# Kernel optimization log

Measured on AMD Instinct MI355X. Metric: run time of the kernel, lower is better.

Reference implementation:

```python
import jax, jax.numpy as jnp
import numpy as np

N_E = 8192
E_DIM = 256
BETA = 0.25


def setup_inputs() -> dict:
    key = jax.random.key(0)
    kz, ke = jax.random.split(key)
    z = jax.random.normal(kz, (16, E_DIM, 32, 32), dtype=jnp.float32)
    embedding = jax.random.uniform(ke, (N_E, E_DIM), dtype=jnp.float32,
                                   minval=-1.0 / N_E, maxval=1.0 / N_E)
    return {"z": z, "embedding": embedding}


def reference(z, embedding):
    n_e, e_dim = embedding.shape
    # (B, C, H, W) -> (B, H, W, C) -> (N, e_dim)
    zp = jnp.transpose(z, (0, 2, 3, 1))
    zf = zp.reshape(-1, e_dim)
    # squared L2 distances: |z|^2 + |e|^2 - 2 z.e   -> (N, n_e)
    dists = (jnp.sum(zf * zf, axis=1, keepdims=True)
             + jnp.sum(embedding * embedding, axis=1)
             - 2.0 * (zf @ embedding.T))
    # two smallest distances (top-2 of negated dists)
    _, top2_idx = jax.lax.top_k(-dists, 2)
    min_encoding_indices = top2_idx[:, 0:1]
    second_encoding_indices = top2_idx[:, 1:2]
    min_encodings = jax.nn.one_hot(top2_idx[:, 0], n_e, dtype=zp.dtype)  # (N, n_e)
    z_q = (min_encodings @ embedding).reshape(zp.shape)
    # commitment / codebook loss
    loss = (jnp.mean((jax.lax.stop_gradient(z_q) - zp) ** 2)
            + BETA * jnp.mean((z_q - jax.lax.stop_gradient(zp)) ** 2))
    # straight-through estimator
    z_q = zp + jax.lax.stop_gradient(z_q - zp)
    avg_probs = jnp.mean(min_encodings, axis=0)
    perplexity = jnp.exp(-jnp.sum(avg_probs * jnp.log(avg_probs + 1e-10)))
    z_q = jnp.transpose(z_q, (0, 3, 1, 2))
    return (loss, z_q, perplexity, min_encodings,
            min_encoding_indices, second_encoding_indices)
```

## Files before the change

kernel.cpp:

```cpp
#include <hip/hip_runtime.h>
#include <cfloat>
#include <cstdint>
#include <cstddef>

#define M_ROWS 16384
#define NE     8192
#define KD     256

#define OFF_LOSS   0ULL
#define OFF_ZQ     1ULL
#define OFF_PERP   4194305ULL
#define OFF_ONEHOT 4194306ULL
#define OFF_I0     138412034ULL
#define OFF_I1     138428418ULL

#define SCR_Z16  0ULL
#define SCR_E16  2097152ULL
#define SCR_PART 3145728ULL

#define WS_I0    0
#define WS_HIST  16384
#define WS_ENORM 24576
#define WS_CNORM 32768
#define WS_T0SUM 49152
#define WS_TOTAL 49154

typedef _Float16 fp16x8 __attribute__((ext_vector_type(8)));
typedef float    floatx16 __attribute__((ext_vector_type(16)));

__device__ __forceinline__ void async_load16(const void* g, void* lds) {
    __builtin_amdgcn_global_load_lds(
        (const __attribute__((address_space(1))) void*)g,
        (__attribute__((address_space(3))) void*)lds, 16, 0, 0);
}

__global__ void zero_ws_kernel(float* __restrict__ ws) {
    int i = blockIdx.x * 256 + threadIdx.x;
    if (i < WS_TOTAL) ws[i] = 0.0f;
}

__global__ void zero_onehot_kernel(float* __restrict__ out) {
    size_t tidg = (size_t)blockIdx.x * 1024 + threadIdx.x;
    float4* base = (float4*)(out + OFF_ONEHOT + 2);
    const float4 zz = make_float4(0.f, 0.f, 0.f, 0.f);
#pragma unroll
    for (int i = 0; i < 8; i++) {
        size_t q = tidg + (size_t)i * 4194304ULL;
        if (q < 33554431ULL) base[q] = zz;
    }
    if (tidg == 0) {
        out[OFF_ONEHOT + 0] = 0.f;
        out[OFF_ONEHOT + 1] = 0.f;
        out[OFF_ONEHOT + 134217726ULL] = 0.f;
        out[OFF_ONEHOT + 134217727ULL] = 0.f;
    }
}

__global__ void scatter_ones_kernel(const int* __restrict__ ws_i0, float* __restrict__ out) {
    int r = blockIdx.x * 256 + threadIdx.x;
    int j = ws_i0[r] & (NE - 1);
    out[OFF_ONEHOT + (size_t)r * NE + j] = 1.0f;
}

__device__ __forceinline__ float pairwise16(const float* sq, int lane16) {
    const int h = lane16 >> 3;
    const int j = lane16 & 7;
    float r = sq[h * 128 + j];
#pragma unroll
    for (int i = 1; i < 16; i++) r = r + sq[h * 128 + i * 8 + j];
    float s = r + __shfl_xor(r, 1);
    s = s + __shfl_xor(s, 2);
    s = s + __shfl_xor(s, 4);
    s = s + __shfl_xor(s, 8);
    return s;
}

__global__ void enorm_kernel(const float* __restrict__ emb, float* __restrict__ enorm) {
    __shared__ float sq[16][257];
    const int tid = threadIdx.x;
    const int row0 = blockIdx.x * 16;
#pragma unroll
    for (int p = 0; p < 4; p++) {
        int q = p * 256 + tid;
        int rl = q >> 6, kq = q & 63;
        float4 v = *(const float4*)(emb + (size_t)(row0 + rl) * KD + kq * 4);
        sq[rl][kq * 4 + 0] = v.x * v.x;
        sq[rl][kq * 4 + 1] = v.y * v.y;
        sq[rl][kq * 4 + 2] = v.z * v.z;
        sq[rl][kq * 4 + 3] = v.w * v.w;
    }
    __syncthreads();
    const int rl = tid >> 4, lane16 = tid & 15;
    float s = pairwise16(&sq[rl][0], lane16);
    if (lane16 == 0) enorm[row0 + rl] = s;
}

__global__ void cnorm_kernel(const float* __restrict__ z, float* __restrict__ cnorm) {
    __shared__ float sq[16][257];
    const int tid = threadIdx.x;
    const int r0  = blockIdx.x * 16;
    const int b   = r0 >> 10;
    const int hw0 = r0 & 1023;
    const float* zb = z + ((size_t)b << 18) + hw0;
#pragma unroll
    for (int p = 0; p < 4; p++) {
        int q = p * 256 + tid;
        int c = q >> 2, hq = q & 3;
        float4 v = *(const float4*)(zb + ((size_t)c << 10) + hq * 4);
        sq[hq * 4 + 0][c] = v.x * v.x;
        sq[hq * 4 + 1][c] = v.y * v.y;
        sq[hq * 4 + 2][c] = v.z * v.z;
        sq[hq * 4 + 3][c] = v.w * v.w;
    }
    __syncthreads();
    const int rl = tid >> 4, lane16 = tid & 15;
    float s = pairwise16(&sq[rl][0], lane16);
    if (lane16 == 0) cnorm[r0 + rl] = s;
}

__global__ void split_z_kernel(const float* __restrict__ z, _Float16* __restrict__ z16) {
    __shared__ float tile[64][65];
    const int tid = threadIdx.x;
    const int r0  = blockIdx.x * 64;
    const int kb  = blockIdx.y;
    const int b   = r0 >> 10;
    const int hw0 = r0 & 1023;
#pragma unroll
    for (int p = 0; p < 4; p++) {
        int q = p * 256 + tid;
        int cl = q >> 4, hq = q & 15;
        float4 v = *(const float4*)(z + ((size_t)b << 18) + (size_t)(kb * 64 + cl) * 1024 + hw0 + hq * 4);
        tile[hq * 4 + 0][cl] = v.x;
        tile[hq * 4 + 1][cl] = v.y;
        tile[hq * 4 + 2][cl] = v.z;
        tile[hq * 4 + 3][cl] = v.w;
    }
    __syncthreads();
#pragma unroll
    for (int p = 0; p < 2; p++) {
        int u = p * 256 + tid;
        int row = u >> 3, k8 = u & 7;
        int r = r0 + row;
        fp16x8 vh;
#pragma unroll
        for (int e = 0; e < 8; e++) vh[e] = (_Float16)tile[row][k8 * 8 + e];
        size_t unit = ((size_t)(r >> 7) * 4 + kb) * 1024 + (size_t)(r & 127) * 8 + (k8 ^ (r & 7));
        *(fp16x8*)(z16 + unit * 8) = vh;
    }
}

__global__ void split_e_kernel(const float* __restrict__ emb, _Float16* __restrict__ e16) {
    int u = blockIdx.x * 256 + threadIdx.x;
    size_t go = (size_t)u * 8;
    float4 v0 = *(const float4*)(emb + go);
    float4 v1 = *(const float4*)(emb + go + 4);
    float x[8] = {v0.x, v0.y, v0.z, v0.w, v1.x, v1.y, v1.z, v1.w};
    fp16x8 vh;
#pragma unroll
    for (int e = 0; e < 8; e++) vh[e] = (_Float16)(x[e] * 256.0f);
    int code = u >> 5, kc = (u >> 3) & 3, ku8 = u & 7;
    int kj = ku8 ^ (code & 7);
    size_t unit = ((size_t)(code >> 7) * 4 + kc) * 1024 + (size_t)(code & 127) * 8 + kj;
    *(fp16x8*)(e16 + unit * 8) = vh;
}

__device__ __forceinline__ void stage16k(_Float16* lds, const _Float16* gsrc,
                                         int wid, int lane) {
#pragma unroll
    for (int p = 0; p < 4; p++) {
        int u = p * 256 + wid * 64;
        async_load16((const void*)(gsrc + (size_t)(u + lane) * 8),
                     (void*)(lds + (size_t)u * 8));
    }
}

__device__ __forceinline__ fp16x8 frag_ld(const _Float16* lds, int rc, int ku) {
    int slot = rc * 8 + (ku ^ (rc & 7));
    return *(const fp16x8*)(lds + slot * 8);
}

#define MFMA(d, a, b) d = __builtin_amdgcn_mfma_f32_32x32x16_f16(a, b, d, 0, 0, 0)

__device__ __forceinline__ bool lex_lt(float t, int i, float T, int I) {
    return (t < T) || (t == T && i < I);
}

__device__ __forceinline__ void ins4(float t, int i,
    float& t0, int& i0, float& t1, int& i1,
    float& t2, int& i2, float& t3, int& i3) {
    if (lex_lt(t, i, t3, i3)) {
        if (lex_lt(t, i, t2, i2)) {
            t3 = t2; i3 = i2;
            if (lex_lt(t, i, t1, i1)) {
                t2 = t1; i2 = i1;
                if (lex_lt(t, i, t0, i0)) { t1 = t0; i1 = i0; t0 = t; i0 = i; }
                else { t1 = t; i1 = i; }
            } else { t2 = t; i2 = i; }
        } else { t3 = t; i3 = i; }
    }
}

__launch_bounds__(256, 2)
__global__ void mfma_top4_kernel(const _Float16* __restrict__ e16, const _Float16* __restrict__ z16,
                                 const float* __restrict__ enorm_g, const float* __restrict__ cnorm_g,
                                 float4* __restrict__ part) {
    __shared__ _Float16 As[2][8192];
    __shared__ _Float16 Bs[2][8192];
    __shared__ float en_all[1024];
    __shared__ float mbuf[128][8];

    const int tid = threadIdx.x;
    const int lane = tid & 63, wid = tid >> 6;
    const int l31 = lane & 31, half = lane >> 5;
    const int wave_m = wid & 1, wave_n = wid >> 1;
    const int zb = blockIdx.x, jg = blockIdx.y;
    const int brow0 = zb * 128;

    const int rcA0 = wave_m * 64 + l31, rcA1 = rcA0 + 32;
    const int rcB0 = wave_n * 64 + l31, rcB1 = rcB0 + 32;

#pragma unroll
    for (int p = 0; p < 4; p++) en_all[p * 256 + tid] = enorm_g[jg * 1024 + p * 256 + tid];

    float Cn[2];
    Cn[0] = cnorm_g[brow0 + wave_n * 64 + l31];
    Cn[1] = cnorm_g[brow0 + wave_n * 64 + 32 + l31];

    float q0[2], q1[2], q2[2], q3[2];
    int   j0[2], j1[2], j2[2], j3[2];
#pragma unroll
    for (int s = 0; s < 2; s++) {
        q0[s] = q1[s] = q2[s] = q3[s] = FLT_MAX;
        j0[s] = j1[s] = j2[s] = j3[s] = 0x7fffffff;
    }

    stage16k(As[0], e16 + ((size_t)((jg * 8 + 0) * 4 + 0) * 1024) * 8, wid, lane);
    stage16k(Bs[0], z16 + ((size_t)(zb * 4 + 0) * 1024) * 8, wid, lane);
    __syncthreads();

    floatx16 acc00, acc01, acc10, acc11;
    for (int iter = 0; iter < 32; iter++) {
        const int jt = iter >> 2, kc = iter & 3;
        const int cur = iter & 1;
        if (kc == 0) {
            acc00 = (floatx16)0.f; acc01 = (floatx16)0.f;
            acc10 = (floatx16)0.f; acc11 = (floatx16)0.f;
        }
        if (iter < 31) {
            const int ni = iter + 1, njt = ni >> 2, nkc = ni & 3;
            stage16k(As[cur ^ 1], e16 + ((size_t)((jg * 8 + njt) * 4 + nkc) * 1024) * 8, wid, lane);
            stage16k(Bs[cur ^ 1], z16 + ((size_t)(zb * 4 + nkc) * 1024) * 8, wid, lane);
        }
#pragma unroll
        for (int ks = 0; ks < 4; ks++) {
            const int ku = ks * 2 + half;
            fp16x8 a0 = frag_ld(As[cur], rcA0, ku);
            fp16x8 a1 = frag_ld(As[cur], rcA1, ku);
            fp16x8 b0 = frag_ld(Bs[cur], rcB0, ku);
            fp16x8 b1 = frag_ld(Bs[cur], rcB1, ku);
            MFMA(acc00, a0, b0);
            MFMA(acc01, a0, b1);
            MFMA(acc10, a1, b0);
            MFMA(acc11, a1, b1);
        }
        if (kc == 3) {
            const int jbase = jg * 1024 + jt * 128;
#pragma unroll
            for (int a = 0; a < 2; a++) {
#pragma unroll
                for (int reg = 0; reg < 16; reg++) {
                    const int rl = (reg & 3) + 8 * (reg >> 2) + 4 * half;
                    const int cl = wave_m * 64 + a * 32 + rl;
                    const int code = jbase + cl;
                    const float E = en_all[jt * 128 + cl];
                    float g0 = (a == 0) ? acc00[reg] : acc10[reg];
                    float g1 = (a == 0) ? acc01[reg] : acc11[reg];
                    float ta = fmaf(-0.0078125f, g0, Cn[0] + E);
                    ins4(ta, code, q0[0], j0[0], q1[0], j1[0], q2[0], j2[0], q3[0], j3[0]);
                    float tb = fmaf(-0.0078125f, g1, Cn[1] + E);
                    ins4(tb, code, q0[1], j0[1], q1[1], j1[1], q2[1], j2[1], q3[1], j3[1]);
                }
            }
        }
        __syncthreads();
    }

#pragma unroll
    for (int s = 0; s < 2; s++) {
        float ot0 = __shfl_xor(q0[s], 32), ot1 = __shfl_xor(q1[s], 32),
              ot2 = __shfl_xor(q2[s], 32), ot3 = __shfl_xor(q3[s], 32);
        int oi0 = __shfl_xor(j0[s], 32), oi1 = __shfl_xor(j1[s], 32),
            oi2 = __shfl_xor(j2[s], 32), oi3 = __shfl_xor(j3[s], 32);
        ins4(ot0, oi0, q0[s], j0[s], q1[s], j1[s], q2[s], j2[s], q3[s], j3[s]);
        ins4(ot1, oi1, q0[s], j0[s], q1[s], j1[s], q2[s], j2[s], q3[s], j3[s]);
        ins4(ot2, oi2, q0[s], j0[s], q1[s], j1[s], q2[s], j2[s], q3[s], j3[s]);
        ins4(ot3, oi3, q0[s], j0[s], q1[s], j1[s], q2[s], j2[s], q3[s], j3[s]);
    }

    __syncthreads();
    if (wave_m == 1 && lane < 32) {
#pragma unroll
        for (int s = 0; s < 2; s++) {
            int zr = wave_n * 64 + s * 32 + l31;
            mbuf[zr][0] = q0[s]; mbuf[zr][1] = q1[s]; mbuf[zr][2] = q2[s]; mbuf[zr][3] = q3[s];
            mbuf[zr][4] = __int_as_float(j0[s]); mbuf[zr][5] = __int_as_float(j1[s]);
            mbuf[zr][6] = __int_as_float(j2[s]); mbuf[zr][7] = __int_as_float(j3[s]);
        }
    }
    __syncthreads();
    if (wave_m == 0 && lane < 32) {
#pragma unroll
        for (int s = 0; s < 2; s++) {
            int zr = wave_n * 64 + s * 32 + l31;
            ins4(mbuf[zr][0], __float_as_int(mbuf[zr][4]),
                 q0[s], j0[s], q1[s], j1[s], q2[s], j2[s], q3[s], j3[s]);
            ins4(mbuf[zr][1], __float_as_int(mbuf[zr][5]),
                 q0[s], j0[s], q1[s], j1[s], q2[s], j2[s], q3[s], j3[s]);
            ins4(mbuf[zr][2], __float_as_int(mbuf[zr][6]),
                 q0[s], j0[s], q1[s], j1[s], q2[s], j2[s], q3[s], j3[s]);
            ins4(mbuf[zr][3], __float_as_int(mbuf[zr][7]),
                 q0[s], j0[s], q1[s], j1[s], q2[s], j2[s], q3[s], j3[s]);
            float4 pa = make_float4(q0[s], q1[s], q2[s], q3[s]);
            float4 pb = make_float4(__int_as_float(j0[s]), __int_as_float(j1[s]),
                                    __int_as_float(j2[s]), __int_as_float(j3[s]));
            size_t base = ((size_t)(brow0 + zr) * 8 + jg) * 2;
            part[base] = pa;
            part[base + 1] = pb;
        }
    }
}

__global__ void rescore_kernel(const float* __restrict__ z, const float* __restrict__ emb,
                               const float* __restrict__ enorm_g, const float* __restrict__ cnorm_g,
                               const float4* __restrict__ part, float* __restrict__ out,
                               int* __restrict__ ws_i0, int* __restrict__ hist,
                               double* __restrict__ t0sum) {
    const int tid  = threadIdx.x;
    const int lane = tid & 63, wid = tid >> 6;
    const int r = blockIdx.x * 4 + wid;
    const int b = r >> 10, hw = r & 1023;
    const float* zb = z + ((size_t)b << 18) + hw;

    const int c4 = lane * 4;
    const double zv0 = (double)zb[(size_t)(c4 + 0) << 10];
    const double zv1 = (double)zb[(size_t)(c4 + 1) << 10];
    const double zv2 = (double)zb[(size_t)(c4 + 2) << 10];
    const double zv3 = (double)zb[(size_t)(c4 + 3) << 10];

    float m1 = FLT_MAX, m2 = FLT_MAX;
    for (int jg = 0; jg < 8; jg++) {
        float4 pa = part[((size_t)r * 8 + jg) * 2];
        if (pa.x < m1) { m2 = m1; m1 = pa.x; } else if (pa.x < m2) m2 = pa.x;
        if (pa.y < m1) { m2 = m1; m1 = pa.y; } else if (pa.y < m2) m2 = pa.y;
    }
    const float T = m2 + 1.2e-4f;
    const float C = cnorm_g[r];

    float bt0 = FLT_MAX, bt1 = FLT_MAX;
    int   bi0 = NE - 1, bi1 = NE - 1;
    bool  any = false;
    for (int jg = 0; jg < 8; jg++) {
        float4 pa = part[((size_t)r * 8 + jg) * 2];
        float4 pb = part[((size_t)r * 8 + jg) * 2 + 1];
        float tv[4] = {pa.x, pa.y, pa.z, pa.w};
        int   jv[4] = {__float_as_int(pb.x), __float_as_int(pb.y),
                       __float_as_int(pb.z), __float_as_int(pb.w)};
        for (int e = 0; e < 4; e++) {
            if (tv[e] <= T) {
                const int j = jv[e] & (NE - 1);
                const float* er = emb + ((size_t)j << 8);
                float4 ev = *(const float4*)(er + c4);
                double gl = zv0 * (double)ev.x + zv1 * (double)ev.y +
                            zv2 * (double)ev.z + zv3 * (double)ev.w;
#pragma unroll
                for (int m = 1; m < 64; m <<= 1) gl += __shfl_xor(gl, m);
                float g2 = (float)(2.0 * gl);
                float S = C + enorm_g[j];
                float tex = S - g2;
                if (tex < bt0 || (tex == bt0 && j < bi0)) {
                    bt1 = bt0; bi1 = bi0; bt0 = tex; bi0 = j;
                } else if (tex < bt1 || (tex == bt1 && j < bi1)) {
                    bt1 = tex; bi1 = j;
                }
                any = true;
            }
        }
    }
    if (!any) { bt0 = 0.f; bi0 = 0; bi1 = 0; }

    if (lane == 0) {
        out[OFF_I0 + r] = (float)bi0;
        out[OFF_I1 + r] = (float)bi1;
        ws_i0[r] = bi0;
        atomicAdd(&hist[bi0], 1);
    }
    __shared__ double red[4];
    if (lane == 0) red[wid] = (double)bt0;
    __syncthreads();
    if (tid == 0) atomicAdd(t0sum, (red[0] + red[1]) + (red[2] + red[3]));
}

__global__ void zq_kernel(const float* __restrict__ emb, const int* __restrict__ ws_i0,
                          float* __restrict__ out) {
    int bc = blockIdx.x;
    int bb = bc >> 8, c = bc & 255;
    int hwb = threadIdx.x * 4;
    const int4 iv = *(const int4*)(ws_i0 + bb * 1024 + hwb);
    float* op = out + OFF_ZQ + ((size_t)bc << 10) + hwb;
    op[0] = emb[(size_t)(iv.x & (NE - 1)) * KD + c];
    op[1] = emb[(size_t)(iv.y & (NE - 1)) * KD + c];
    op[2] = emb[(size_t)(iv.z & (NE - 1)) * KD + c];
    op[3] = emb[(size_t)(iv.w & (NE - 1)) * KD + c];
}

__global__ void finalize_kernel(const int* __restrict__ hist, const double* __restrict__ t0sum,
                                float* __restrict__ out) {
    __shared__ float red[256];
    float s = 0.f;
    for (int j = threadIdx.x; j < NE; j += 256) {
        float p = (float)hist[j] * (1.0f / 16384.0f);
        s += p * logf(p + 1e-10f);
    }
    red[threadIdx.x] = s;
    __syncthreads();
    for (int m = 128; m; m >>= 1) {
        if (threadIdx.x < m) red[threadIdx.x] += red[threadIdx.x + m];
        __syncthreads();
    }
    if (threadIdx.x == 0) {
        out[OFF_PERP] = expf(-red[0]);
        out[OFF_LOSS] = 1.25f * (float)(t0sum[0] * (1.0 / 4194304.0));
    }
}

extern "C" void kernel_launch(void* const* d_in, const int* in_sizes, int n_in,
                              void* d_out, int out_size, void* d_ws, size_t ws_size,
                              hipStream_t stream) {
    const float* z   = (const float*)d_in[0];
    const float* emb = (const float*)d_in[1];
    float* out = (float*)d_out;
    float* ws  = (float*)d_ws;

    int*    ws_i0    = (int*)ws + WS_I0;
    int*    ws_hist  = (int*)ws + WS_HIST;
    float*  ws_enorm = ws + WS_ENORM;
    float*  ws_cnorm = ws + WS_CNORM;
    double* ws_t0sum = (double*)(ws + WS_T0SUM);

    float* scr = out + OFF_ONEHOT + 2;
    _Float16* z16 = (_Float16*)(scr + SCR_Z16);
    _Float16* e16 = (_Float16*)(scr + SCR_E16);
    float4* part = (float4*)(scr + SCR_PART);

    hipLaunchKernelGGL(zero_ws_kernel, dim3(194), dim3(256), 0, stream, ws);
    hipLaunchKernelGGL(enorm_kernel, dim3(512), dim3(256), 0, stream, emb, ws_enorm);
    hipLaunchKernelGGL(cnorm_kernel, dim3(1024), dim3(256), 0, stream, z, ws_cnorm);
    hipLaunchKernelGGL(split_z_kernel, dim3(256, 4), dim3(256), 0, stream, z, z16);
    hipLaunchKernelGGL(split_e_kernel, dim3(1024), dim3(256), 0, stream, emb, e16);
    hipLaunchKernelGGL(mfma_top4_kernel, dim3(128, 8), dim3(256), 0, stream,
                       e16, z16, ws_enorm, ws_cnorm, part);
    hipLaunchKernelGGL(rescore_kernel, dim3(4096), dim3(256), 0, stream,
                       z, emb, ws_enorm, ws_cnorm, part, out, ws_i0, ws_hist, ws_t0sum);
    hipLaunchKernelGGL(zero_onehot_kernel, dim3(4096), dim3(1024), 0, stream, out);
    hipLaunchKernelGGL(scatter_ones_kernel, dim3(64), dim3(256), 0, stream, ws_i0, out);
    hipLaunchKernelGGL(zq_kernel, dim3(4096), dim3(256), 0, stream, emb, ws_i0, out);
    hipLaunchKernelGGL(finalize_kernel, dim3(1), dim3(256), 0, stream,
                       ws_hist, ws_t0sum, out);
}
```

Measured before the change: 1.306 ms.

## Keep full z tile resident in LDS, transpose z for rescore, tile zq writes

The MFMA top-4 kernel now runs 512-thread blocks that load a block's whole 128x256 fp16 z tile into LDS once and stream only codebook tiles through double buffers. Each wave covers 32 z rows instead of 64, so it carries one top-4 state. split_z also writes a row-major fp32 copy of z so the rescore kernel can read it with float4 loads instead of strided gathers. zq is rewritten to gather codebook rows coalesced and transpose them through LDS for coalesced NCHW stores. The trade is more LDS per block, a lower per-wave MFMA-to-load ratio, and extra scratch writes.

```diff
diff --git a/kernel.cpp b/kernel.cpp
--- a/kernel.cpp
+++ b/kernel.cpp
@@ -17,6 +17,7 @@
 #define SCR_Z16  0ULL
 #define SCR_E16  2097152ULL
 #define SCR_PART 3145728ULL
+#define SCR_Z32T 4194304ULL
 
 #define WS_I0    0
 #define WS_HIST  16384
@@ -118,7 +119,8 @@
     if (lane16 == 0) cnorm[r0 + rl] = s;
 }
 
-__global__ void split_z_kernel(const float* __restrict__ z, _Float16* __restrict__ z16) {
+__global__ void split_z_kernel(const float* __restrict__ z, _Float16* __restrict__ z16,
+                               float* __restrict__ z32t) {
     __shared__ float tile[64][65];
     const int tid = threadIdx.x;
     const int r0  = blockIdx.x * 64;
@@ -146,6 +148,13 @@
         for (int e = 0; e < 8; e++) vh[e] = (_Float16)tile[row][k8 * 8 + e];
         size_t unit = ((size_t)(r >> 7) * 4 + kb) * 1024 + (size_t)(r & 127) * 8 + (k8 ^ (r & 7));
         *(fp16x8*)(z16 + unit * 8) = vh;
+    }
+#pragma unroll
+    for (int p = 0; p < 4; p++) {
+        int q = p * 256 + tid;
+        int row = q >> 4, co = (q & 15) * 4;
+        float4 v = make_float4(tile[row][co], tile[row][co + 1], tile[row][co + 2], tile[row][co + 3]);
+        *(float4*)(z32t + (size_t)(r0 + row) * 256 + kb * 64 + co) = v;
     }
 }
 
@@ -162,16 +171,6 @@
     int kj = ku8 ^ (code & 7);
     size_t unit = ((size_t)(code >> 7) * 4 + kc) * 1024 + (size_t)(code & 127) * 8 + kj;
     *(fp16x8*)(e16 + unit * 8) = vh;
-}
-
-__device__ __forceinline__ void stage16k(_Float16* lds, const _Float16* gsrc,
-                                         int wid, int lane) {
-#pragma unroll
-    for (int p = 0; p < 4; p++) {
-        int u = p * 256 + wid * 64;
-        async_load16((const void*)(gsrc + (size_t)(u + lane) * 8),
-                     (void*)(lds + (size_t)u * 8));
-    }
 }
 
 __device__ __forceinline__ fp16x8 frag_ld(const _Float16* lds, int rc, int ku) {
@@ -200,12 +199,12 @@
     }
 }
 
-__launch_bounds__(256, 2)
+__launch_bounds__(512, 1)
 __global__ void mfma_top4_kernel(const _Float16* __restrict__ e16, const _Float16* __restrict__ z16,
                                  const float* __restrict__ enorm_g, const float* __restrict__ cnorm_g,
                                  float4* __restrict__ part) {
-    __shared__ _Float16 As[2][8192];
-    __shared__ _Float16 Bs[2][8192];
+    __shared__ _Float16 Zs[32768];
+    __shared__ _Float16 Es[2][8192];
     __shared__ float en_all[1024];
     __shared__ float mbuf[128][8];
 
@@ -213,55 +212,57 @@
     const int lane = tid & 63, wid = tid >> 6;
     const int l31 = lane & 31, half = lane >> 5;
     const int wave_m = wid & 1, wave_n = wid >> 1;
-    const int zb = blockIdx.x, jg = blockIdx.y;
+    const int jg = blockIdx.x, zb = blockIdx.y;
     const int brow0 = zb * 128;
 
     const int rcA0 = wave_m * 64 + l31, rcA1 = rcA0 + 32;
-    const int rcB0 = wave_n * 64 + l31, rcB1 = rcB0 + 32;
-
-#pragma unroll
-    for (int p = 0; p < 4; p++) en_all[p * 256 + tid] = enorm_g[jg * 1024 + p * 256 + tid];
-
-    float Cn[2];
-    Cn[0] = cnorm_g[brow0 + wave_n * 64 + l31];
-    Cn[1] = cnorm_g[brow0 + wave_n * 64 + 32 + l31];
-
-    float q0[2], q1[2], q2[2], q3[2];
-    int   j0[2], j1[2], j2[2], j3[2];
-#pragma unroll
-    for (int s = 0; s < 2; s++) {
-        q0[s] = q1[s] = q2[s] = q3[s] = FLT_MAX;
-        j0[s] = j1[s] = j2[s] = j3[s] = 0x7fffffff;
-    }
-
-    stage16k(As[0], e16 + ((size_t)((jg * 8 + 0) * 4 + 0) * 1024) * 8, wid, lane);
-    stage16k(Bs[0], z16 + ((size_t)(zb * 4 + 0) * 1024) * 8, wid, lane);
-    __syncthreads();
-
-    floatx16 acc00, acc01, acc10, acc11;
+    const int rcB  = wave_n * 32 + l31;
+
+#pragma unroll
+    for (int p = 0; p < 2; p++) en_all[p * 512 + tid] = enorm_g[jg * 1024 + p * 512 + tid];
+
+    const float Cn = cnorm_g[brow0 + rcB];
+
+#pragma unroll
+    for (int p = 0; p < 8; p++) {
+        int ub = p * 512 + wid * 64;
+        async_load16((const void*)(z16 + ((size_t)zb * 4096 + ub + lane) * 8),
+                     (void*)(Zs + (size_t)ub * 8));
+    }
+#pragma unroll
+    for (int p = 0; p < 2; p++) {
+        int ub = p * 512 + wid * 64;
+        async_load16((const void*)(e16 + ((size_t)(jg * 8 + 0) * 4096 + ub + lane) * 8),
+                     (void*)(Es[0] + (size_t)ub * 8));
+    }
+    __syncthreads();
+
+    float q0 = FLT_MAX, q1 = FLT_MAX, q2 = FLT_MAX, q3 = FLT_MAX;
+    int   j0 = 0x7fffffff, j1 = 0x7fffffff, j2 = 0x7fffffff, j3 = 0x7fffffff;
+
+    floatx16 acc0, acc1;
     for (int iter = 0; iter < 32; iter++) {
         const int jt = iter >> 2, kc = iter & 3;
         const int cur = iter & 1;
-        if (kc == 0) {
-            acc00 = (floatx16)0.f; acc01 = (floatx16)0.f;
-            acc10 = (floatx16)0.f; acc11 = (floatx16)0.f;
-        }
+        if (kc == 0) { acc0 = (floatx16)0.f; acc1 = (floatx16)0.f; }
         if (iter < 31) {
             const int ni = iter + 1, njt = ni >> 2, nkc = ni & 3;
-            stage16k(As[cur ^ 1], e16 + ((size_t)((jg * 8 + njt) * 4 + nkc) * 1024) * 8, wid, lane);
-            stage16k(Bs[cur ^ 1], z16 + ((size_t)(zb * 4 + nkc) * 1024) * 8, wid, lane);
+#pragma unroll
+            for (int p = 0; p < 2; p++) {
+                int ub = p * 512 + wid * 64;
+                async_load16((const void*)(e16 + ((size_t)((jg * 8 + njt) * 4 + nkc) * 1024 + ub + lane) * 8),
+                             (void*)(Es[cur ^ 1] + (size_t)ub * 8));
+            }
         }
+        const _Float16* zsec = Zs + kc * 8192;
 #pragma unroll
         for (int ks = 0; ks < 4; ks++) {
             const int ku = ks * 2 + half;
-            fp16x8 a0 = frag_ld(As[cur], rcA0, ku);
-            fp16x8 a1 = frag_ld(As[cur], rcA1, ku);
-            fp16x8 b0 = frag_ld(Bs[cur], rcB0, ku);
-            fp16x8 b1 = frag_ld(Bs[cur], rcB1, ku);
-            MFMA(acc00, a0, b0);
-            MFMA(acc01, a0, b1);
-            MFMA(acc10, a1, b0);
-            MFMA(acc11, a1, b1);
+            fp16x8 a0 = frag_ld(Es[cur], rcA0, ku);
+            fp16x8 a1 = frag_ld(Es[cur], rcA1, ku);
+            fp16x8 b0 = frag_ld(zsec, rcB, ku);
+            MFMA(acc0, a0, b0);
+            MFMA(acc1, a1, b0);
         }
         if (kc == 3) {
             const int jbase = jg * 1024 + jt * 128;
@@ -273,64 +274,50 @@
                     const int cl = wave_m * 64 + a * 32 + rl;
                     const int code = jbase + cl;
                     const float E = en_all[jt * 128 + cl];
-                    float g0 = (a == 0) ? acc00[reg] : acc10[reg];
-                    float g1 = (a == 0) ? acc01[reg] : acc11[reg];
-                    float ta = fmaf(-0.0078125f, g0, Cn[0] + E);
-                    ins4(ta, code, q0[0], j0[0], q1[0], j1[0], q2[0], j2[0], q3[0], j3[0]);
-                    float tb = fmaf(-0.0078125f, g1, Cn[1] + E);
-                    ins4(tb, code, q0[1], j0[1], q1[1], j1[1], q2[1], j2[1], q3[1], j3[1]);
+                    float g = (a == 0) ? acc0[reg] : acc1[reg];
+                    float t = fmaf(-0.0078125f, g, Cn + E);
+                    ins4(t, code, q0, j0, q1, j1, q2, j2, q3, j3);
                 }
             }
         }
         __syncthreads();
     }
 
-#pragma unroll
-    for (int s = 0; s < 2; s++) {
-        float ot0 = __shfl_xor(q0[s], 32), ot1 = __shfl_xor(q1[s], 32),
-              ot2 = __shfl_xor(q2[s], 32), ot3 = __shfl_xor(q3[s], 32);
-        int oi0 = __shfl_xor(j0[s], 32), oi1 = __shfl_xor(j1[s], 32),
-            oi2 = __shfl_xor(j2[s], 32), oi3 = __shfl_xor(j3[s], 32);
-        ins4(ot0, oi0, q0[s], j0[s], q1[s], j1[s], q2[s], j2[s], q3[s], j3[s]);
-        ins4(ot1, oi1, q0[s], j0[s], q1[s], j1[s], q2[s], j2[s], q3[s], j3[s]);
-        ins4(ot2, oi2, q0[s], j0[s], q1[s], j1[s], q2[s], j2[s], q3[s], j3[s]);
-        ins4(ot3, oi3, q0[s], j0[s], q1[s], j1[s], q2[s], j2[s], q3[s], j3[s]);
+    {
+        float ot0 = __shfl_xor(q0, 32), ot1 = __shfl_xor(q1, 32),
+              ot2 = __shfl_xor(q2, 32), ot3 = __shfl_xor(q3, 32);
+        int oi0 = __shfl_xor(j0, 32), oi1 = __shfl_xor(j1, 32),
+            oi2 = __shfl_xor(j2, 32), oi3 = __shfl_xor(j3, 32);
+        ins4(ot0, oi0, q0, j0, q1, j1, q2, j2, q3, j3);
+        ins4(ot1, oi1, q0, j0, q1, j1, q2, j2, q3, j3);
+        ins4(ot2, oi2, q0, j0, q1, j1, q2, j2, q3, j3);
+        ins4(ot3, oi3, q0, j0, q1, j1, q2, j2, q3, j3);
     }
 
     __syncthreads();
     if (wave_m == 1 && lane < 32) {
-#pragma unroll
-        for (int s = 0; s < 2; s++) {
-            int zr = wave_n * 64 + s * 32 + l31;
-            mbuf[zr][0] = q0[s]; mbuf[zr][1] = q1[s]; mbuf[zr][2] = q2[s]; mbuf[zr][3] = q3[s];
-            mbuf[zr][4] = __int_as_float(j0[s]); mbuf[zr][5] = __int_as_float(j1[s]);
-            mbuf[zr][6] = __int_as_float(j2[s]); mbuf[zr][7] = __int_as_float(j3[s]);
-        }
+        int zr = wave_n * 32 + l31;
+        mbuf[zr][0] = q0; mbuf[zr][1] = q1; mbuf[zr][2] = q2; mbuf[zr][3] = q3;
+        mbuf[zr][4] = __int_as_float(j0); mbuf[zr][5] = __int_as_float(j1);
+        mbuf[zr][6] = __int_as_float(j2); mbuf[zr][7] = __int_as_float(j3);
     }
     __syncthreads();
     if (wave_m == 0 && lane < 32) {
-#pragma unroll
-        for (int s = 0; s < 2; s++) {
-            int zr = wave_n * 64 + s * 32 + l31;
-            ins4(mbuf[zr][0], __float_as_int(mbuf[zr][4]),
-                 q0[s], j0[s], q1[s], j1[s], q2[s], j2[s], q3[s], j3[s]);
-            ins4(mbuf[zr][1], __float_as_int(mbuf[zr][5]),
-                 q0[s], j0[s], q1[s], j1[s], q2[s], j2[s], q3[s], j3[s]);
-            ins4(mbuf[zr][2], __float_as_int(mbuf[zr][6]),
-                 q0[s], j0[s], q1[s], j1[s], q2[s], j2[s], q3[s], j3[s]);
-            ins4(mbuf[zr][3], __float_as_int(mbuf[zr][7]),
-                 q0[s], j0[s], q1[s], j1[s], q2[s], j2[s], q3[s], j3[s]);
-            float4 pa = make_float4(q0[s], q1[s], q2[s], q3[s]);
-            float4 pb = make_float4(__int_as_float(j0[s]), __int_as_float(j1[s]),
-                                    __int_as_float(j2[s]), __int_as_float(j3[s]));
-            size_t base = ((size_t)(brow0 + zr) * 8 + jg) * 2;
-            part[base] = pa;
-            part[base + 1] = pb;
-        }
-    }
-}
-
-__global__ void rescore_kernel(const float* __restrict__ z, const float* __restrict__ emb,
+        int zr = wave_n * 32 + l31;
+        ins4(mbuf[zr][0], __float_as_int(mbuf[zr][4]), q0, j0, q1, j1, q2, j2, q3, j3);
+        ins4(mbuf[zr][1], __float_as_int(mbuf[zr][5]), q0, j0, q1, j1, q2, j2, q3, j3);
+        ins4(mbuf[zr][2], __float_as_int(mbuf[zr][6]), q0, j0, q1, j1, q2, j2, q3, j3);
+        ins4(mbuf[zr][3], __float_as_int(mbuf[zr][7]), q0, j0, q1, j1, q2, j2, q3, j3);
+        float4 pa = make_float4(q0, q1, q2, q3);
+        float4 pb = make_float4(__int_as_float(j0), __int_as_float(j1),
+                                __int_as_float(j2), __int_as_float(j3));
+        size_t base = ((size_t)(brow0 + zr) * 8 + jg) * 2;
+        part[base] = pa;
+        part[base + 1] = pb;
+    }
+}
+
+__global__ void rescore_kernel(const float* __restrict__ z32t, const float* __restrict__ emb,
                                const float* __restrict__ enorm_g, const float* __restrict__ cnorm_g,
                                const float4* __restrict__ part, float* __restrict__ out,
                                int* __restrict__ ws_i0, int* __restrict__ hist,
@@ -338,14 +325,10 @@
     const int tid  = threadIdx.x;
     const int lane = tid & 63, wid = tid >> 6;
     const int r = blockIdx.x * 4 + wid;
-    const int b = r >> 10, hw = r & 1023;
-    const float* zb = z + ((size_t)b << 18) + hw;
 
     const int c4 = lane * 4;
-    const double zv0 = (double)zb[(size_t)(c4 + 0) << 10];
-    const double zv1 = (double)zb[(size_t)(c4 + 1) << 10];
-    const double zv2 = (double)zb[(size_t)(c4 + 2) << 10];
-    const double zv3 = (double)zb[(size_t)(c4 + 3) << 10];
+    float4 zv = *(const float4*)(z32t + (size_t)r * 256 + c4);
+    const double zv0 = (double)zv.x, zv1 = (double)zv.y, zv2 = (double)zv.z, zv3 = (double)zv.w;
 
     float m1 = FLT_MAX, m2 = FLT_MAX;
     for (int jg = 0; jg < 8; jg++) {
@@ -368,8 +351,7 @@
         for (int e = 0; e < 4; e++) {
             if (tv[e] <= T) {
                 const int j = jv[e] & (NE - 1);
-                const float* er = emb + ((size_t)j << 8);
-                float4 ev = *(const float4*)(er + c4);
+                float4 ev = *(const float4*)(emb + ((size_t)j << 8) + c4);
                 double gl = zv0 * (double)ev.x + zv1 * (double)ev.y +
                             zv2 * (double)ev.z + zv3 * (double)ev.w;
 #pragma unroll
@@ -402,15 +384,29 @@
 
 __global__ void zq_kernel(const float* __restrict__ emb, const int* __restrict__ ws_i0,
                           float* __restrict__ out) {
-    int bc = blockIdx.x;
-    int bb = bc >> 8, c = bc & 255;
-    int hwb = threadIdx.x * 4;
-    const int4 iv = *(const int4*)(ws_i0 + bb * 1024 + hwb);
-    float* op = out + OFF_ZQ + ((size_t)bc << 10) + hwb;
-    op[0] = emb[(size_t)(iv.x & (NE - 1)) * KD + c];
-    op[1] = emb[(size_t)(iv.y & (NE - 1)) * KD + c];
-    op[2] = emb[(size_t)(iv.z & (NE - 1)) * KD + c];
-    op[3] = emb[(size_t)(iv.w & (NE - 1)) * KD + c];
+    __shared__ float zt[64][65];
+    const int tid = threadIdx.x;
+    const int r0  = blockIdx.x * 64;
+    const int b   = r0 >> 10;
+    const int hw0 = r0 & 1023;
+    const int kb  = blockIdx.y;
+#pragma unroll
+    for (int p = 0; p < 4; p++) {
+        int q = p * 256 + tid;
+        int row = q >> 4, co = (q & 15) * 4;
+        int idx = ws_i0[r0 + row] & (NE - 1);
+        float4 v = *(const float4*)(emb + ((size_t)idx << 8) + kb * 64 + co);
+        zt[row][co + 0] = v.x; zt[row][co + 1] = v.y;
+        zt[row][co + 2] = v.z; zt[row][co + 3] = v.w;
+    }
+    __syncthreads();
+#pragma unroll
+    for (int p = 0; p < 4; p++) {
+        int q = p * 256 + tid;
+        int c = q >> 4, h4 = (q & 15) * 4;
+        float4 v = make_float4(zt[h4 + 0][c], zt[h4 + 1][c], zt[h4 + 2][c], zt[h4 + 3][c]);
+        *(float4*)(out + OFF_ZQ + (((size_t)b * 256 + kb * 64 + c) << 10) + hw0 + h4) = v;
+    }
 }
 
 __global__ void finalize_kernel(const int* __restrict__ hist, const double* __restrict__ t0sum,
@@ -450,20 +446,21 @@
     float* scr = out + OFF_ONEHOT + 2;
     _Float16* z16 = (_Float16*)(scr + SCR_Z16);
     _Float16* e16 = (_Float16*)(scr + SCR_E16);
-    float4* part = (float4*)(scr + SCR_PART);
+    float4* part  = (float4*)(scr + SCR_PART);
+    float*  z32t  = scr + SCR_Z32T;
 
     hipLaunchKernelGGL(zero_ws_kernel, dim3(194), dim3(256), 0, stream, ws);
     hipLaunchKernelGGL(enorm_kernel, dim3(512), dim3(256), 0, stream, emb, ws_enorm);
     hipLaunchKernelGGL(cnorm_kernel, dim3(1024), dim3(256), 0, stream, z, ws_cnorm);
-    hipLaunchKernelGGL(split_z_kernel, dim3(256, 4), dim3(256), 0, stream, z, z16);
+    hipLaunchKernelGGL(split_z_kernel, dim3(256, 4), dim3(256), 0, stream, z, z16, z32t);
     hipLaunchKernelGGL(split_e_kernel, dim3(1024), dim3(256), 0, stream, emb, e16);
-    hipLaunchKernelGGL(mfma_top4_kernel, dim3(128, 8), dim3(256), 0, stream,
+    hipLaunchKernelGGL(mfma_top4_kernel, dim3(8, 128), dim3(512), 0, stream,
                        e16, z16, ws_enorm, ws_cnorm, part);
     hipLaunchKernelGGL(rescore_kernel, dim3(4096), dim3(256), 0, stream,
-                       z, emb, ws_enorm, ws_cnorm, part, out, ws_i0, ws_hist, ws_t0sum);
+                       z32t, emb, ws_enorm, ws_cnorm, part, out, ws_i0, ws_hist, ws_t0sum);
     hipLaunchKernelGGL(zero_onehot_kernel, dim3(4096), dim3(1024), 0, stream, out);
     hipLaunchKernelGGL(scatter_ones_kernel, dim3(64), dim3(256), 0, stream, ws_i0, out);
-    hipLaunchKernelGGL(zq_kernel, dim3(4096), dim3(256), 0, stream, emb, ws_i0, out);
+    hipLaunchKernelGGL(zq_kernel, dim3(256, 4), dim3(256), 0, stream, emb, ws_i0, out);
     hipLaunchKernelGGL(finalize_kernel, dim3(1), dim3(256), 0, stream,
                        ws_hist, ws_t0sum, out);
 }
```

New measurement: 1.342 ms. +2.7%, slower.
